# Kernel optimization log

Hardware: AMD Instinct MI355X
Metric: run time of the kernel (lower is better)

## Reference

```python
import jax, jax.numpy as jnp
import numpy as np

B, T, C, H = 2, 2048, 1024, 16  # batch, seq (== block_size), n_embd, n_head
HD = C // H  # head dim


def setup_inputs() -> dict:
    key = jax.random.key(0)
    k1, k2, k3 = jax.random.split(key, 3)
    x = jax.random.normal(k1, (B, T, C), dtype=jnp.float32)
    w_attn = jax.random.normal(k2, (C, 3 * C), dtype=jnp.float32) * (1.0 / np.sqrt(C))
    b_attn = jnp.zeros((3 * C,), dtype=jnp.float32)
    w_proj = jax.random.normal(k3, (C, C), dtype=jnp.float32) * (1.0 / np.sqrt(C))
    b_proj = jnp.zeros((C,), dtype=jnp.float32)
    return {"x": x, "w_attn": w_attn, "b_attn": b_attn, "w_proj": w_proj, "b_proj": b_proj}


def reference(x, w_attn, b_attn, w_proj, b_proj):
    # qkv projection: [B,T,3C]
    qkv = x @ w_attn + b_attn
    q, k, v = jnp.split(qkv, 3, axis=-1)
    # -> [B,H,T,HD]
    def to_heads(t):
        return t.reshape(B, T, H, HD).transpose(0, 2, 1, 3)
    q, k, v = to_heads(q), to_heads(k), to_heads(v)
    scale = 1.0 / np.sqrt(HD).astype(np.float32)
    # att: [B,H,T,T]
    att = jnp.einsum("bhqd,bhkd->bhqk", q, k) * scale
    causal = jnp.tril(jnp.ones((T, T), dtype=bool))
    att = jnp.where(causal[None, None], att, -jnp.inf)
    att = jax.nn.softmax(att, axis=-1)
    # y: [B,H,T,HD] -> [B,T,C]
    y = jnp.einsum("bhqk,bhkd->bhqd", att, v)
    y = y.transpose(0, 2, 1, 3).reshape(B, T, C)
    return y @ w_proj + b_proj
```

## Files before the change

### kernel.cpp

```cpp
#include <hip/hip_runtime.h>
#include <stdint.h>

#define Bb 2
#define Tt 2048
#define Cc 1024
#define Hh 16
#define HD 64
#define C3 3072

typedef __bf16 bf16x8 __attribute__((ext_vector_type(8)));
typedef float  f32x4  __attribute__((ext_vector_type(4)));
typedef unsigned short u16;
typedef u16 u16x8 __attribute__((ext_vector_type(8)));
typedef u16 u16x4 __attribute__((ext_vector_type(4)));

#define SCALE2 0.18033688f

__device__ __forceinline__ u16 f2bf(float f) {
  union { float f; unsigned u; } v; v.f = f;
  return (u16)((v.u + 0x7fffu + ((v.u >> 16) & 1u)) >> 16);
}
__device__ __forceinline__ float bf2f(u16 a) {
  union { unsigned u; float f; } v; v.u = ((unsigned)a) << 16; return v.f;
}

__device__ __forceinline__ void gl2lds16(const void* g, void* s) {
  __builtin_amdgcn_global_load_lds(
      (__attribute__((address_space(1))) void*)(g),
      (__attribute__((address_space(3))) void*)(s), 16, 0, 0);
}

__device__ __forceinline__ bf16x8 ldb8(const u16* p) {
  return __builtin_bit_cast(bf16x8, *(const u16x8*)p);
}

__global__ __launch_bounds__(256)
void prep_kernel(const float* __restrict__ x, const float* __restrict__ w_attn,
                 const float* __restrict__ w_proj, u16* __restrict__ xb,
                 u16* __restrict__ wat, u16* __restrict__ wpt) {
  __shared__ u16 tile[64][65];
  const int blk = blockIdx.x;
  const int tid = threadIdx.x;
  if (blk < 4096) {
    int i = blk * 256 + tid;
    float4 v = ((const float4*)x)[i];
    u16x4 o = { f2bf(v.x), f2bf(v.y), f2bf(v.z), f2bf(v.w) };
    ((u16x4*)xb)[i] = o;
    return;
  }
  const float* in; u16* out; int R, C, c0, r0;
  if (blk < 4096 + 768) {
    int t = blk - 4096;
    in = w_attn; out = wat; R = 1024; C = 3072;
    c0 = (t % 48) * 64; r0 = (t / 48) * 64;
  } else {
    int t = blk - 4864;
    in = w_proj; out = wpt; R = 1024; C = 1024;
    c0 = (t & 15) * 64; r0 = (t >> 4) * 64;
  }
  int xx = tid & 63, yy = tid >> 6;
  #pragma unroll
  for (int rr = yy; rr < 64; rr += 4)
    tile[rr][xx] = f2bf(in[(size_t)(r0 + rr) * C + c0 + xx]);
  __syncthreads();
  #pragma unroll
  for (int rr = yy; rr < 64; rr += 4)
    out[(size_t)(c0 + rr) * R + r0 + xx] = tile[xx][rr];
}

template <int MODE, int BN>
__global__ __launch_bounds__(256, 4)
void gemm_bt(const u16* __restrict__ A, const u16* __restrict__ Bt,
             const float* __restrict__ bias, void* __restrict__ Cout,
             u16* __restrict__ Vt, int M, int N, int K) {
  __shared__ u16 As[2][128 * 32];
  __shared__ u16 Bs[2][BN * 32];
  constexpr int JT = BN / 32;
  const int tid = threadIdx.x;
  const int ln  = tid & 63;
  const int w   = tid >> 6;
  const int wm  = w >> 1, wn = w & 1;
  const int l15 = ln & 15, lq = ln >> 4;
  const int swz2 = (l15 >> 1) & 3;
  const int m0 = blockIdx.y * 128, n0 = blockIdx.x * BN;

  int aoff[2], boff[BN / 128 + 1];
  #pragma unroll
  for (int i = 0; i < 2; ++i) {
    int s = i * 256 + tid;
    int row = s >> 2, cg = (s & 3) ^ ((s >> 3) & 3);
    aoff[i] = (m0 + row) * K + cg * 8;
  }
  #pragma unroll
  for (int i = 0; i < BN / 128 + 1; ++i) {
    int s = i * 256 + tid;
    int row = s >> 2, cg = (s & 3) ^ ((s >> 3) & 3);
    boff[i] = (n0 + row) * K + cg * 8;
  }

  f32x4 acc[4][JT];
  #pragma unroll
  for (int i = 0; i < 4; ++i)
    #pragma unroll
    for (int j = 0; j < JT; ++j)
      acc[i][j] = (f32x4){0.f, 0.f, 0.f, 0.f};

  const int NK = K >> 5;
  #pragma unroll
  for (int i = 0; i < 2; ++i)
    gl2lds16(A + aoff[i], (char*)As[0] + (size_t)(i * 256 + w * 64) * 16);
  #pragma unroll
  for (int i = 0; i < BN / 128 + 1; ++i)
    gl2lds16(Bt + boff[i], (char*)Bs[0] + (size_t)(i * 256 + w * 64) * 16);

  for (int it = 0; it < NK; ++it) {
    const int p = it & 1;
    __syncthreads();
    if (it + 1 < NK) {
      const int k0 = (it + 1) * 32;
      #pragma unroll
      for (int i = 0; i < 2; ++i)
        gl2lds16(A + aoff[i] + k0, (char*)As[p ^ 1] + (size_t)(i * 256 + w * 64) * 16);
      #pragma unroll
      for (int i = 0; i < BN / 128 + 1; ++i)
        gl2lds16(Bt + boff[i] + k0, (char*)Bs[p ^ 1] + (size_t)(i * 256 + w * 64) * 16);
    }
    const u16* AsB = As[p];
    const u16* BsB = Bs[p];
    bf16x8 af[4], bfr[JT];
    #pragma unroll
    for (int i = 0; i < 4; ++i)
      af[i] = ldb8(&AsB[(wm * 64 + i * 16 + l15) * 32 + ((lq ^ swz2) * 8)]);
    #pragma unroll
    for (int j = 0; j < JT; ++j)
      bfr[j] = ldb8(&BsB[(wn * (BN / 2) + j * 16 + l15) * 32 + ((lq ^ swz2) * 8)]);
    #pragma unroll
    for (int i = 0; i < 4; ++i)
      #pragma unroll
      for (int j = 0; j < JT; ++j)
        acc[i][j] = __builtin_amdgcn_mfma_f32_16x16x32_bf16(af[i], bfr[j], acc[i][j], 0, 0, 0);
  }

  if (MODE == 1 && n0 >= 2048) {
    #pragma unroll
    for (int i = 0; i < 4; ++i) {
      int rowb = m0 + wm * 64 + i * 16 + lq * 4;
      int b_ = rowb >> 11, t0 = rowb & 2047;
      int tl = t0 & 63;
      int c = tl >> 4, ll = (tl >> 2) & 3;
      int pos0 = (c >> 1) * 32 + ll * 8 + (c & 1) * 4;
      size_t tdst = (size_t)(t0 & ~63) + pos0;
      #pragma unroll
      for (int j = 0; j < JT; ++j) {
        int col = n0 + wn * (BN / 2) + j * 16 + l15;
        int hd = col - 2048;
        float bsv = bias[col];
        u16x4 pk;
        #pragma unroll
        for (int r = 0; r < 4; ++r) pk[r] = f2bf(acc[i][j][r] + bsv);
        *(u16x4*)&Vt[(size_t)(b_ * 1024 + hd) * Tt + tdst] = pk;
      }
    }
  } else {
    const int ldc = (MODE == 1) ? 2048 : N;
    #pragma unroll
    for (int i = 0; i < 4; ++i) {
      int row = m0 + wm * 64 + i * 16 + lq * 4;
      #pragma unroll
      for (int j = 0; j < JT; ++j) {
        int col = n0 + wn * (BN / 2) + j * 16 + l15;
        float bsv = bias[col];
        #pragma unroll
        for (int r = 0; r < 4; ++r) {
          float v = acc[i][j][r] + bsv;
          if (MODE == 1) ((u16*)Cout)[(size_t)(row + r) * ldc + col] = f2bf(v);
          else           ((float*)Cout)[(size_t)(row + r) * ldc + col] = v;
        }
      }
    }
  }
}


__device__ __forceinline__ bf16x8 packp(const f32x4& a, const f32x4& b) {
  bf16x8 r;
  #pragma unroll
  for (int i = 0; i < 4; ++i) { r[i] = (__bf16)a[i]; r[i + 4] = (__bf16)b[i]; }
  return r;
}
__device__ __forceinline__ bf16x8 qscale(const u16* p) {
  u16x8 q = *(const u16x8*)p;
  u16x8 s;
  #pragma unroll
  for (int j = 0; j < 8; ++j) s[j] = f2bf(bf2f(q[j]) * SCALE2);
  return __builtin_bit_cast(bf16x8, s);
}

__device__ __forceinline__ void softmax_step(f32x4 (&t)[4], float& m, f32x4 (&o)[4],
                                             f32x4& lacc, bool maskDiag, int kk,
                                             int qg, int lq) {
  if (maskDiag) {
    #pragma unroll
    for (int i = 0; i < 4; ++i)
      #pragma unroll
      for (int r = 0; r < 4; ++r) {
        int kv = kk + i * 16 + lq * 4 + r;
        if (kv > qg) t[i][r] = -__builtin_inff();
      }
  }
  float a0 = fmaxf(fmaxf(t[0][0], t[0][1]), fmaxf(t[0][2], t[0][3]));
  float a1 = fmaxf(fmaxf(t[1][0], t[1][1]), fmaxf(t[1][2], t[1][3]));
  float a2 = fmaxf(fmaxf(t[2][0], t[2][1]), fmaxf(t[2][2], t[2][3]));
  float a3 = fmaxf(fmaxf(t[3][0], t[3][1]), fmaxf(t[3][2], t[3][3]));
  float mx = fmaxf(fmaxf(a0, a1), fmaxf(a2, a3));
  mx = fmaxf(mx, __shfl_xor(mx, 16));
#if __has_builtin(__builtin_amdgcn_permlane32_swap)
  {
    unsigned mu = __builtin_bit_cast(unsigned, mx);
    auto r2 = __builtin_amdgcn_permlane32_swap(mu, mu, false, false);
    mx = fmaxf(__builtin_bit_cast(float, (unsigned)r2[0]),
               __builtin_bit_cast(float, (unsigned)r2[1]));
  }
#else
  mx = fmaxf(mx, __shfl_xor(mx, 32));
#endif
  if (!__all(mx <= m + 8.0f)) {
    float mn = fmaxf(m, mx);
    float al = __builtin_amdgcn_exp2f(m - mn);
    m = mn;
    lacc[0] *= al;
    #pragma unroll
    for (int jd = 0; jd < 4; ++jd)
      #pragma unroll
      for (int r = 0; r < 4; ++r) o[jd][r] *= al;
  }
  #pragma unroll
  for (int i = 0; i < 4; ++i)
    #pragma unroll
    for (int r = 0; r < 4; ++r)
      t[i][r] = __builtin_amdgcn_exp2f(t[i][r] - m);
}

__global__ __launch_bounds__(256, 2)
void attn_fused(const u16* __restrict__ qk, const u16* __restrict__ vt,
                u16* __restrict__ y) {
  __shared__ u16 Ks[2][64 * 64];
  __shared__ u16 Vts[2][64 * 64];
  const int tid = threadIdx.x;
  const int ln = tid & 63, w = tid >> 6;
  const int l15 = ln & 15, lq = ln >> 4;
  const int swz = l15 & 7;
  const int bx = blockIdx.x;
  const int bh = bx & 31;
  const int h  = bh & 15, b = bh >> 4;
  const int g  = (bx >> 5) & 7;
  const int pr = (bx < 256) ? g : 15 - g;
  const int qtA = 31 - pr, qtB = pr;

  const u16* qbase = qk + (size_t)(b * Tt) * 2048 + h * HD;
  const u16* kbase = qk + (size_t)(b * Tt) * 2048 + 1024 + h * HD;
  const u16* vbase = vt + (size_t)(b * 1024 + h * HD) * Tt;

  const int s0 = tid, s1 = 256 + tid;
  const int koff0 = (s0 >> 3) * 2048 + (((s0 & 7) ^ ((s0 >> 3) & 7)) * 8);
  const int koff1 = (s1 >> 3) * 2048 + (((s1 & 7) ^ ((s1 >> 3) & 7)) * 8);

  const int q0A = qtA * 64 + w * 16;
  const int q0B = qtB * 64 + w * 16;

  const u16* qrA = qbase + (size_t)(q0A + l15) * 2048;
  const u16* qrB = qbase + (size_t)(q0B + l15) * 2048;
  bf16x8 qA0 = qscale(qrA + lq * 8), qA1 = qscale(qrA + 32 + lq * 8);
  bf16x8 qB0 = qscale(qrB + lq * 8), qB1 = qscale(qrB + 32 + lq * 8);

  bf16x8 ones;
  #pragma unroll
  for (int j = 0; j < 8; ++j) ones[j] = (__bf16)1.0f;

  f32x4 oA[4], oB[4];
  #pragma unroll
  for (int j = 0; j < 4; ++j) { oA[j] = (f32x4){0, 0, 0, 0}; oB[j] = (f32x4){0, 0, 0, 0}; }
  f32x4 laccA = (f32x4){0, 0, 0, 0}, laccB = (f32x4){0, 0, 0, 0};
  float mA = -__builtin_inff(), mB = -__builtin_inff();
  const int qgA = q0A + l15, qgB = q0B + l15;

  const int itLast = qtA;

  gl2lds16(kbase + koff0, (char*)Ks[0] + w * 1024);
  gl2lds16(kbase + koff1, (char*)Ks[0] + 4096 + w * 1024);
  gl2lds16(vbase + koff0, (char*)Vts[0] + w * 1024);
  gl2lds16(vbase + koff1, (char*)Vts[0] + 4096 + w * 1024);

  for (int it = 0; it <= itLast; ++it) {
    const int kk = it * 64;
    const int p = it & 1;
    __syncthreads();
    if (it < itLast) {
      const u16* ksrc = kbase + (size_t)(kk + 64) * 2048;
      const u16* vsrc = vbase + kk + 64;
      gl2lds16(ksrc + koff0, (char*)Ks[p ^ 1] + w * 1024);
      gl2lds16(ksrc + koff1, (char*)Ks[p ^ 1] + 4096 + w * 1024);
      gl2lds16(vsrc + koff0, (char*)Vts[p ^ 1] + w * 1024);
      gl2lds16(vsrc + koff1, (char*)Vts[p ^ 1] + 4096 + w * 1024);
    }
    const u16* KsB  = Ks[p];
    const u16* VtsB = Vts[p];
    const bool actB = (it <= qtB);

    f32x4 tA[4], tB[4];
    #pragma unroll
    for (int i = 0; i < 4; ++i) { tA[i] = (f32x4){0, 0, 0, 0}; tB[i] = (f32x4){0, 0, 0, 0}; }
    __builtin_amdgcn_s_setprio(1);
    #pragma unroll
    for (int i = 0; i < 4; ++i) {
      bf16x8 kf0 = ldb8(&KsB[(i * 16 + l15) * 64 + ((lq    ) ^ swz) * 8]);
      bf16x8 kf1 = ldb8(&KsB[(i * 16 + l15) * 64 + ((lq + 4) ^ swz) * 8]);
      tA[i] = __builtin_amdgcn_mfma_f32_16x16x32_bf16(kf0, qA0, tA[i], 0, 0, 0);
      tA[i] = __builtin_amdgcn_mfma_f32_16x16x32_bf16(kf1, qA1, tA[i], 0, 0, 0);
      if (actB) {
        tB[i] = __builtin_amdgcn_mfma_f32_16x16x32_bf16(kf0, qB0, tB[i], 0, 0, 0);
        tB[i] = __builtin_amdgcn_mfma_f32_16x16x32_bf16(kf1, qB1, tB[i], 0, 0, 0);
      }
    }
    __builtin_amdgcn_s_setprio(0);

    softmax_step(tA, mA, oA, laccA, it == itLast, kk, qgA, lq);
    bf16x8 pA0 = packp(tA[0], tA[1]), pA1 = packp(tA[2], tA[3]);
    bf16x8 pB0 = {}, pB1 = {};
    if (actB) {
      softmax_step(tB, mB, oB, laccB, it == qtB, kk, qgB, lq);
      pB0 = packp(tB[0], tB[1]); pB1 = packp(tB[2], tB[3]);
    }

    __builtin_amdgcn_s_setprio(1);
    #pragma unroll
    for (int mf = 0; mf < 2; ++mf) {
      bf16x8 pa = mf ? pA1 : pA0;
      bf16x8 pb = mf ? pB1 : pB0;
      laccA = __builtin_amdgcn_mfma_f32_16x16x32_bf16(ones, pa, laccA, 0, 0, 0);
      if (actB)
        laccB = __builtin_amdgcn_mfma_f32_16x16x32_bf16(ones, pb, laccB, 0, 0, 0);
      #pragma unroll
      for (int jd = 0; jd < 4; ++jd) {
        int d = jd * 16 + l15;
        bf16x8 vf = ldb8(&VtsB[d * 64 + ((mf * 4 + lq) ^ swz) * 8]);
        oA[jd] = __builtin_amdgcn_mfma_f32_16x16x32_bf16(vf, pa, oA[jd], 0, 0, 0);
        if (actB)
          oB[jd] = __builtin_amdgcn_mfma_f32_16x16x32_bf16(vf, pb, oB[jd], 0, 0, 0);
      }
    }
    __builtin_amdgcn_s_setprio(0);
  }

  {
    float inv = 1.f / laccA[0];
    const size_t ybase = (size_t)(b * Tt + q0A + l15) * Cc + h * HD;
    #pragma unroll
    for (int jd = 0; jd < 4; ++jd) {
      u16x4 pk;
      #pragma unroll
      for (int r = 0; r < 4; ++r) pk[r] = f2bf(oA[jd][r] * inv);
      *(u16x4*)&y[ybase + jd * 16 + lq * 4] = pk;
    }
  }
  {
    float inv = 1.f / laccB[0];
    const size_t ybase = (size_t)(b * Tt + q0B + l15) * Cc + h * HD;
    #pragma unroll
    for (int jd = 0; jd < 4; ++jd) {
      u16x4 pk;
      #pragma unroll
      for (int r = 0; r < 4; ++r) pk[r] = f2bf(oB[jd][r] * inv);
      *(u16x4*)&y[ybase + jd * 16 + lq * 4] = pk;
    }
  }
}

extern "C" void kernel_launch(void* const* d_in, const int* in_sizes, int n_in,
                              void* d_out, int out_size, void* d_ws, size_t ws_size,
                              hipStream_t stream) {
  const float* x      = (const float*)d_in[0];
  const float* w_attn = (const float*)d_in[1];
  const float* b_attn = (const float*)d_in[2];
  const float* w_proj = (const float*)d_in[3];
  const float* b_proj = (const float*)d_in[4];
  float* out = (float*)d_out;

  char* ws = (char*)d_ws;
  u16* xb  = (u16*)(ws + 0);
  u16* wat = (u16*)(ws + 8388608);
  u16* wpt = (u16*)(ws + 14680064);
  u16* qkb = (u16*)(ws + 16777216);
  u16* vtb = (u16*)(ws + 33554432);
  u16* yb  = (u16*)(ws + 41943040);

  prep_kernel<<<5120, 256, 0, stream>>>(x, w_attn, w_proj, xb, wat, wpt);
  gemm_bt<1, 128><<<dim3(24, 32), 256, 0, stream>>>(xb, wat, b_attn, (void*)qkb, vtb, 4096, 3072, 1024);
  attn_fused<<<512, 256, 0, stream>>>(qkb, vtb, yb);
  gemm_bt<0, 64><<<dim3(16, 32), 256, 0, stream>>>(yb, wpt, b_proj, (void*)out, nullptr, 4096, 1024, 1024);
}
```

Baseline: 186.7 us.

## Assign each attention block a contiguous 128-row query tile instead of paired tiles

Each attention block used to pair a late 64-row query tile with an early one, which balanced causal work across blocks. Now each block takes two adjacent 64-row tiles that form one contiguous 128-row span, so every staged K/V tile feeds both halves and fewer K/V loads happen in total. The cost is a wide spread in per-block work: the last blocks run about twice the MFMA work of the old balanced blocks. That can lengthen the critical path when all blocks run at once.

```diff
diff --git a/kernel.cpp b/kernel.cpp
--- a/kernel.cpp
+++ b/kernel.cpp
@@ -254,8 +254,8 @@
   const int bh = bx & 31;
   const int h  = bh & 15, b = bh >> 4;
   const int g  = (bx >> 5) & 7;
-  const int pr = (bx < 256) ? g : 15 - g;
-  const int qtA = 31 - pr, qtB = pr;
+  const int qb = (bx < 256) ? g : 15 - g;
+  const int q0 = qb * 128;
 
   const u16* qbase = qk + (size_t)(b * Tt) * 2048 + h * HD;
   const u16* kbase = qk + (size_t)(b * Tt) * 2048 + 1024 + h * HD;
@@ -265,26 +265,26 @@
   const int koff0 = (s0 >> 3) * 2048 + (((s0 & 7) ^ ((s0 >> 3) & 7)) * 8);
   const int koff1 = (s1 >> 3) * 2048 + (((s1 & 7) ^ ((s1 >> 3) & 7)) * 8);
 
-  const int q0A = qtA * 64 + w * 16;
-  const int q0B = qtB * 64 + w * 16;
-
-  const u16* qrA = qbase + (size_t)(q0A + l15) * 2048;
-  const u16* qrB = qbase + (size_t)(q0B + l15) * 2048;
-  bf16x8 qA0 = qscale(qrA + lq * 8), qA1 = qscale(qrA + 32 + lq * 8);
-  bf16x8 qB0 = qscale(qrB + lq * 8), qB1 = qscale(qrB + 32 + lq * 8);
+  const int rLo = q0 + w * 16;
+  const int rHi = q0 + 64 + w * 16;
+
+  const u16* qrL = qbase + (size_t)(rLo + l15) * 2048;
+  const u16* qrH = qbase + (size_t)(rHi + l15) * 2048;
+  bf16x8 qL0 = qscale(qrL + lq * 8), qL1 = qscale(qrL + 32 + lq * 8);
+  bf16x8 qH0 = qscale(qrH + lq * 8), qH1 = qscale(qrH + 32 + lq * 8);
 
   bf16x8 ones;
   #pragma unroll
   for (int j = 0; j < 8; ++j) ones[j] = (__bf16)1.0f;
 
-  f32x4 oA[4], oB[4];
-  #pragma unroll
-  for (int j = 0; j < 4; ++j) { oA[j] = (f32x4){0, 0, 0, 0}; oB[j] = (f32x4){0, 0, 0, 0}; }
-  f32x4 laccA = (f32x4){0, 0, 0, 0}, laccB = (f32x4){0, 0, 0, 0};
-  float mA = -__builtin_inff(), mB = -__builtin_inff();
-  const int qgA = q0A + l15, qgB = q0B + l15;
-
-  const int itLast = qtA;
+  f32x4 oL[4], oH[4];
+  #pragma unroll
+  for (int j = 0; j < 4; ++j) { oL[j] = (f32x4){0, 0, 0, 0}; oH[j] = (f32x4){0, 0, 0, 0}; }
+  f32x4 laccL = (f32x4){0, 0, 0, 0}, laccH = (f32x4){0, 0, 0, 0};
+  float mL = -__builtin_inff(), mH = -__builtin_inff();
+  const int qgL = rLo + l15, qgH = rHi + l15;
+  const int diagLo = 2 * qb;
+  const int itLast = 2 * qb + 1;
 
   gl2lds16(kbase + koff0, (char*)Ks[0] + w * 1024);
   gl2lds16(kbase + koff1, (char*)Ks[0] + 4096 + w * 1024);
@@ -305,72 +305,72 @@
     }
     const u16* KsB  = Ks[p];
     const u16* VtsB = Vts[p];
-    const bool actB = (it <= qtB);
-
-    f32x4 tA[4], tB[4];
-    #pragma unroll
-    for (int i = 0; i < 4; ++i) { tA[i] = (f32x4){0, 0, 0, 0}; tB[i] = (f32x4){0, 0, 0, 0}; }
+    const bool actLo = (it <= diagLo);
+
+    f32x4 tL[4], tH[4];
+    #pragma unroll
+    for (int i = 0; i < 4; ++i) { tL[i] = (f32x4){0, 0, 0, 0}; tH[i] = (f32x4){0, 0, 0, 0}; }
     __builtin_amdgcn_s_setprio(1);
     #pragma unroll
     for (int i = 0; i < 4; ++i) {
       bf16x8 kf0 = ldb8(&KsB[(i * 16 + l15) * 64 + ((lq    ) ^ swz) * 8]);
       bf16x8 kf1 = ldb8(&KsB[(i * 16 + l15) * 64 + ((lq + 4) ^ swz) * 8]);
-      tA[i] = __builtin_amdgcn_mfma_f32_16x16x32_bf16(kf0, qA0, tA[i], 0, 0, 0);
-      tA[i] = __builtin_amdgcn_mfma_f32_16x16x32_bf16(kf1, qA1, tA[i], 0, 0, 0);
-      if (actB) {
-        tB[i] = __builtin_amdgcn_mfma_f32_16x16x32_bf16(kf0, qB0, tB[i], 0, 0, 0);
-        tB[i] = __builtin_amdgcn_mfma_f32_16x16x32_bf16(kf1, qB1, tB[i], 0, 0, 0);
+      tH[i] = __builtin_amdgcn_mfma_f32_16x16x32_bf16(kf0, qH0, tH[i], 0, 0, 0);
+      tH[i] = __builtin_amdgcn_mfma_f32_16x16x32_bf16(kf1, qH1, tH[i], 0, 0, 0);
+      if (actLo) {
+        tL[i] = __builtin_amdgcn_mfma_f32_16x16x32_bf16(kf0, qL0, tL[i], 0, 0, 0);
+        tL[i] = __builtin_amdgcn_mfma_f32_16x16x32_bf16(kf1, qL1, tL[i], 0, 0, 0);
       }
     }
     __builtin_amdgcn_s_setprio(0);
 
-    softmax_step(tA, mA, oA, laccA, it == itLast, kk, qgA, lq);
-    bf16x8 pA0 = packp(tA[0], tA[1]), pA1 = packp(tA[2], tA[3]);
-    bf16x8 pB0 = {}, pB1 = {};
-    if (actB) {
-      softmax_step(tB, mB, oB, laccB, it == qtB, kk, qgB, lq);
-      pB0 = packp(tB[0], tB[1]); pB1 = packp(tB[2], tB[3]);
-    }
+    bf16x8 pL0 = {}, pL1 = {};
+    if (actLo) {
+      softmax_step(tL, mL, oL, laccL, it == diagLo, kk, qgL, lq);
+      pL0 = packp(tL[0], tL[1]); pL1 = packp(tL[2], tL[3]);
+    }
+    softmax_step(tH, mH, oH, laccH, it == itLast, kk, qgH, lq);
+    bf16x8 pH0 = packp(tH[0], tH[1]), pH1 = packp(tH[2], tH[3]);
 
     __builtin_amdgcn_s_setprio(1);
     #pragma unroll
     for (int mf = 0; mf < 2; ++mf) {
-      bf16x8 pa = mf ? pA1 : pA0;
-      bf16x8 pb = mf ? pB1 : pB0;
-      laccA = __builtin_amdgcn_mfma_f32_16x16x32_bf16(ones, pa, laccA, 0, 0, 0);
-      if (actB)
-        laccB = __builtin_amdgcn_mfma_f32_16x16x32_bf16(ones, pb, laccB, 0, 0, 0);
+      bf16x8 ph = mf ? pH1 : pH0;
+      bf16x8 pl = mf ? pL1 : pL0;
+      laccH = __builtin_amdgcn_mfma_f32_16x16x32_bf16(ones, ph, laccH, 0, 0, 0);
+      if (actLo)
+        laccL = __builtin_amdgcn_mfma_f32_16x16x32_bf16(ones, pl, laccL, 0, 0, 0);
       #pragma unroll
       for (int jd = 0; jd < 4; ++jd) {
         int d = jd * 16 + l15;
         bf16x8 vf = ldb8(&VtsB[d * 64 + ((mf * 4 + lq) ^ swz) * 8]);
-        oA[jd] = __builtin_amdgcn_mfma_f32_16x16x32_bf16(vf, pa, oA[jd], 0, 0, 0);
-        if (actB)
-          oB[jd] = __builtin_amdgcn_mfma_f32_16x16x32_bf16(vf, pb, oB[jd], 0, 0, 0);
+        oH[jd] = __builtin_amdgcn_mfma_f32_16x16x32_bf16(vf, ph, oH[jd], 0, 0, 0);
+        if (actLo)
+          oL[jd] = __builtin_amdgcn_mfma_f32_16x16x32_bf16(vf, pl, oL[jd], 0, 0, 0);
       }
     }
     __builtin_amdgcn_s_setprio(0);
   }
 
   {
-    float inv = 1.f / laccA[0];
-    const size_t ybase = (size_t)(b * Tt + q0A + l15) * Cc + h * HD;
+    float inv = 1.f / laccL[0];
+    const size_t ybase = (size_t)(b * Tt + rLo + l15) * Cc + h * HD;
     #pragma unroll
     for (int jd = 0; jd < 4; ++jd) {
       u16x4 pk;
       #pragma unroll
-      for (int r = 0; r < 4; ++r) pk[r] = f2bf(oA[jd][r] * inv);
+      for (int r = 0; r < 4; ++r) pk[r] = f2bf(oL[jd][r] * inv);
       *(u16x4*)&y[ybase + jd * 16 + lq * 4] = pk;
     }
   }
   {
-    float inv = 1.f / laccB[0];
-    const size_t ybase = (size_t)(b * Tt + q0B + l15) * Cc + h * HD;
+    float inv = 1.f / laccH[0];
+    const size_t ybase = (size_t)(b * Tt + rHi + l15) * Cc + h * HD;
     #pragma unroll
     for (int jd = 0; jd < 4; ++jd) {
       u16x4 pk;
       #pragma unroll
-      for (int r = 0; r < 4; ++r) pk[r] = f2bf(oB[jd][r] * inv);
+      for (int r = 0; r < 4; ++r) pk[r] = f2bf(oH[jd][r] * inv);
       *(u16x4*)&y[ybase + jd * 16 + lq * 4] = pk;
     }
   }
```

Result: faster. 182.7 us (-2.1%).
